# Optimization experiments

Measured on AMD Instinct MI355X. Metric: run time of the kernel, lower is better.

## Reference

```python
import jax, jax.numpy as jnp
import numpy as np

B, N, C, H = 32, 577, 768, 12
D = C // H  # head dim 64
HID = 3072  # hardcoded Mlp hidden
ALPHA = 0.1
EPS = 1e-6


def setup_inputs() -> dict:
    key = jax.random.key(0)
    ks = jax.random.split(key, 8)
    s = 0.02
    return {
        "x": jax.random.normal(ks[0], (B, N, C), jnp.float32),
        "attn_weight": jax.random.uniform(ks[1], (B, N - 1), jnp.float32),
        "ln1_w": jnp.ones((C,), jnp.float32),
        "ln1_b": jnp.zeros((C,), jnp.float32),
        "qkv_w": jax.random.normal(ks[2], (3 * C, C), jnp.float32) * s,
        "qkv_b": jnp.zeros((3 * C,), jnp.float32),
        "proj_w": jax.random.normal(ks[3], (C, C), jnp.float32) * s,
        "proj_b": jnp.zeros((C,), jnp.float32),
        "ln2_w": jnp.ones((C,), jnp.float32),
        "ln2_b": jnp.zeros((C,), jnp.float32),
        "fc1_w": jax.random.normal(ks[4], (HID, C), jnp.float32) * s,
        "fc1_b": jnp.zeros((HID,), jnp.float32),
        "fc2_w": jax.random.normal(ks[5], (C, HID), jnp.float32) * s,
        "fc2_b": jnp.zeros((C,), jnp.float32),
    }


def _ln(x, w, b):
    m = x.mean(-1, keepdims=True)
    v = jnp.var(x, axis=-1, keepdims=True)
    return (x - m) * jax.lax.rsqrt(v + EPS) * w + b


def reference(x, attn_weight, ln1_w, ln1_b, qkv_w, qkv_b, proj_w, proj_b,
              ln2_w, ln2_b, fc1_w, fc1_b, fc2_w, fc2_b):
    h = _ln(x, ln1_w, ln1_b)
    qkv = (h @ qkv_w.T + qkv_b).reshape(B, N, 3, H, D)
    q = qkv[:, :, 0].transpose(0, 2, 1, 3)  # [B,H,N,D]
    k = qkv[:, :, 1].transpose(0, 2, 1, 3)
    v = qkv[:, :, 2].transpose(0, 2, 1, 3)
    scale = D ** -0.5
    attn = jnp.einsum('bhnd,bhmd->bhnm', q, k) * scale  # [B,H,N,N]
    patch_attn = attn[:, :, 0, 1:]  # pre-reweight CLS->patch scores
    # multiplicative reweighting of CLS row (cols 1:) before softmax
    factor = jnp.concatenate(
        [jnp.ones((B, 1), attn.dtype), attn_weight * ALPHA + (1.0 - ALPHA)], axis=-1)
    attn = attn.at[:, :, 0, :].multiply(factor[:, None, :])
    attn = jax.nn.softmax(attn, axis=-1)
    out = jnp.einsum('bhnm,bhmd->bhnd', attn, v)
    out = out.transpose(0, 2, 1, 3).reshape(B, N, C)
    out = out @ proj_w.T + proj_b
    x = x + out
    h2 = _ln(x, ln2_w, ln2_b)
    h2 = jax.nn.gelu(h2 @ fc1_w.T + fc1_b, approximate=False)  # nn.GELU exact
    h2 = h2 @ fc2_w.T + fc2_b
    x = x + h2
    return (x, patch_attn)
```

## Files before the change

kernel.cpp:

```cpp
#include <hip/hip_runtime.h>
#include <hip/hip_bf16.h>
#include <cstdint>

#define BB 32
#define NN 577
#define CC 768
#define HH 12
#define HIDN 3072
#define MROWS (BB*NN)

typedef __attribute__((ext_vector_type(8))) short bf16x8;
typedef __attribute__((ext_vector_type(4))) float f32x4;

__device__ __forceinline__ float b2f(unsigned short u) {
    union { float f; unsigned int i; } x; x.i = ((unsigned int)u) << 16; return x.f;
}
__device__ __forceinline__ unsigned short f2b(float f) {
    union { float f; unsigned int i; } x; x.f = f;
    unsigned int i = x.i;
    i += 0x7fffu + ((i >> 16) & 1u);
    return (unsigned short)(i >> 16);
}

__device__ __forceinline__ void async16(const void* g, void* l) {
    __builtin_amdgcn_global_load_lds(
        (const __attribute__((address_space(1))) uint32_t*)g,
        (__attribute__((address_space(3))) uint32_t*)l, 16, 0, 0);
}

__device__ __forceinline__ float gelu_f(float v) {
    float ax = fabsf(v) * 0.70710678118654752f;
    float t = __builtin_amdgcn_rcpf(1.0f + 0.3275911f * ax);
    float poly = t * (0.254829592f + t * (-0.284496736f + t * (1.421413741f +
                 t * (-1.453152027f + t * 1.061405429f))));
    float e = __expf(-ax * ax);
    float erf_abs = 1.0f - poly * e;
    float erf_v = (v >= 0.f) ? erf_abs : -erf_abs;
    return 0.5f * v * (1.0f + erf_v);
}

__global__ void cvt4(const float* __restrict__ a, int na, unsigned short* __restrict__ oa,
                     const float* __restrict__ b, int nb, unsigned short* __restrict__ ob,
                     const float* __restrict__ c, int nc, unsigned short* __restrict__ oc,
                     const float* __restrict__ d, int nd, unsigned short* __restrict__ od) {
    int stride = gridDim.x * blockDim.x;
    int t = blockIdx.x * blockDim.x + threadIdx.x;
    for (int i = t; i < na; i += stride) oa[i] = f2b(a[i]);
    for (int i = t; i < nb; i += stride) ob[i] = f2b(b[i]);
    for (int i = t; i < nc; i += stride) oc[i] = f2b(c[i]);
    for (int i = t; i < nd; i += stride) od[i] = f2b(d[i]);
}

__global__ __launch_bounds__(256)
void ln_kernel(const float* __restrict__ x, const float* __restrict__ w,
               const float* __restrict__ bsv, unsigned short* __restrict__ out) {
    int row = blockIdx.x;
    const float* xr = x + (size_t)row * CC;
    float v[3]; float s = 0.f, ss = 0.f;
    #pragma unroll
    for (int i = 0; i < 3; ++i) {
        v[i] = xr[threadIdx.x + i * 256];
        s += v[i]; ss += v[i] * v[i];
    }
    int lane = threadIdx.x & 63, wv = threadIdx.x >> 6;
    #pragma unroll
    for (int off = 32; off; off >>= 1) { s += __shfl_down(s, off); ss += __shfl_down(ss, off); }
    __shared__ float rs[4], rss[4];
    __shared__ float mean_s, rstd_s;
    if (lane == 0) { rs[wv] = s; rss[wv] = ss; }
    __syncthreads();
    if (threadIdx.x == 0) {
        float S = rs[0] + rs[1] + rs[2] + rs[3];
        float SS = rss[0] + rss[1] + rss[2] + rss[3];
        float m = S * (1.0f / 768.0f);
        float var = SS * (1.0f / 768.0f) - m * m;
        mean_s = m; rstd_s = rsqrtf(var + 1e-6f);
    }
    __syncthreads();
    float m = mean_s, r = rstd_s;
    #pragma unroll
    for (int i = 0; i < 3; ++i) {
        int c = threadIdx.x + i * 256;
        out[(size_t)row * CC + c] = f2b((v[i] - m) * r * w[c] + bsv[c]);
    }
}

template <int EPI>
__global__ __launch_bounds__(256, 4)
void gemm_bt(const unsigned short* __restrict__ A, const unsigned short* __restrict__ Bw,
             const float* __restrict__ bias, const float* __restrict__ resid,
             unsigned short* __restrict__ outb, float* __restrict__ outf,
             int M, int N, int K) {
    const int NT = gridDim.x;
    const int MT = (M + 127) >> 7;
    int flat = blockIdx.y * NT + blockIdx.x;
    int xcd = flat & 7, s = flat >> 3;
    int n_t = s % NT, mj = s / NT;
    int m_t = xcd + 8 * mj;
    if (m_t >= MT) return;
    const int m0 = m_t * 128, n0 = n_t * 128;

    __shared__ __align__(16) unsigned short As[2][128 * 32];
    __shared__ __align__(16) unsigned short Bs[2][128 * 32];
    const int tid = threadIdx.x;
    const int wave = tid >> 6, lane = tid & 63;
    const int wr = wave >> 1, wc = wave & 1;
    const int quad = lane >> 4, l16 = lane & 15;

    f32x4 acc[4][4] = {};

    const int c0 = tid, c1 = 256 + tid;
    const int row0 = c0 >> 2, seg0 = c0 & 3;
    const int row1 = c1 >> 2, seg1 = c1 & 3;
    int gm0 = m0 + row0; if (gm0 > M - 1) gm0 = M - 1;
    int gm1 = m0 + row1; if (gm1 > M - 1) gm1 = M - 1;
    const unsigned short* a0 = A + (size_t)gm0 * K + seg0 * 8;
    const unsigned short* a1 = A + (size_t)gm1 * K + seg1 * 8;
    const unsigned short* b0 = Bw + (size_t)(n0 + row0) * K + seg0 * 8;
    const unsigned short* b1 = Bw + (size_t)(n0 + row1) * K + seg1 * 8;

    for (int k0 = 0; k0 < K; k0 += 64) {
        #pragma unroll
        for (int p = 0; p < 2; ++p) {
            int kk = k0 + p * 32;
            async16(a0 + kk, &As[p][c0 * 8]);
            async16(a1 + kk, &As[p][c1 * 8]);
            async16(b0 + kk, &Bs[p][c0 * 8]);
            async16(b1 + kk, &Bs[p][c1 * 8]);
        }
        __syncthreads();
        #pragma unroll
        for (int p = 0; p < 2; ++p) {
            bf16x8 bfr[4];
            #pragma unroll
            for (int ni = 0; ni < 4; ++ni)
                bfr[ni] = *(const bf16x8*)&Bs[p][(wc * 64 + ni * 16 + l16) * 32 + quad * 8];
            #pragma unroll
            for (int mi = 0; mi < 4; ++mi) {
                bf16x8 af = *(const bf16x8*)&As[p][(wr * 64 + mi * 16 + l16) * 32 + quad * 8];
                #pragma unroll
                for (int ni = 0; ni < 4; ++ni)
                    acc[mi][ni] = __builtin_amdgcn_mfma_f32_16x16x32_bf16(af, bfr[ni], acc[mi][ni], 0, 0, 0);
            }
        }
        __syncthreads();
    }

    #pragma unroll
    for (int mi = 0; mi < 4; ++mi) {
        #pragma unroll
        for (int r = 0; r < 4; ++r) {
            int grow = m0 + wr * 64 + mi * 16 + quad * 4 + r;
            if (grow >= M) continue;
            #pragma unroll
            for (int ni = 0; ni < 4; ++ni) {
                int gcol = n0 + wc * 64 + ni * 16 + l16;
                float v = acc[mi][ni][r] + bias[gcol];
                size_t idx = (size_t)grow * N + gcol;
                if (EPI == 0) {
                    outb[idx] = f2b(v);
                } else if (EPI == 1) {
                    outb[idx] = f2b(gelu_f(v));
                } else {
                    outf[idx] = resid[idx] + v;
                }
            }
        }
    }
}

__global__ __launch_bounds__(256)
void attn_mfma(const unsigned short* __restrict__ qkv, const float* __restrict__ aw,
               unsigned short* __restrict__ O, float* __restrict__ patch) {
    const int qt = blockIdx.x, h = blockIdx.y, b = blockIdx.z;
    const int tid = threadIdx.x, wv = tid >> 6, lane = tid & 63;
    const int quad = lane >> 4, l16 = lane & 15;

    __shared__ __align__(16) unsigned short Ks[64 * 72];
    __shared__ __align__(16) unsigned short Vt[64 * 72];
    __shared__ __align__(16) unsigned short Pt[4][16 * 72];

    int qrow = qt * 64 + wv * 16 + l16;
    int qclamp = qrow < NN ? qrow : NN - 1;
    const unsigned short* qbase = qkv + (size_t)(b * NN + qclamp) * 2304 + h * 64;
    bf16x8 qf[2];
    qf[0] = *(const bf16x8*)(qbase + quad * 8);
    qf[1] = *(const bf16x8*)(qbase + 32 + quad * 8);
    #pragma unroll
    for (int i = 0; i < 2; ++i) {
        union { bf16x8 v; unsigned short u[8]; } t; t.v = qf[i];
        #pragma unroll
        for (int j = 0; j < 8; ++j) t.u[j] = f2b(b2f(t.u[j]) * 0.125f);
        qf[i] = t.v;
    }

    f32x4 o[4] = {};
    float mst[4], lst[4];
    #pragma unroll
    for (int r = 0; r < 4; ++r) { mst[r] = -1.0e30f; lst[r] = 0.f; }

    for (int kt = 0; kt < 10; ++kt) {
        __syncthreads();
        #pragma unroll
        for (int i = 0; i < 2; ++i) {
            int c = i * 256 + tid;
            int key = c >> 3, seg = c & 7;
            int gk = kt * 64 + key; if (gk >= NN) gk = NN - 1;
            const unsigned short* kb = qkv + (size_t)(b * NN + gk) * 2304 + 768 + h * 64 + seg * 8;
            bf16x8 kv = *(const bf16x8*)kb;
            *(bf16x8*)&Ks[key * 72 + seg * 8] = kv;
            const unsigned short* vb = qkv + (size_t)(b * NN + gk) * 2304 + 1536 + h * 64 + seg * 8;
            bf16x8 vvv = *(const bf16x8*)vb;
            int kg = key >> 3, kl = key & 7;
            int swz = (kg ^ seg) * 8 + kl;
            #pragma unroll
            for (int e = 0; e < 8; ++e)
                Vt[(seg * 8 + e) * 72 + swz] = ((const unsigned short*)&vvv)[e];
        }
        __syncthreads();

        f32x4 s[4];
        #pragma unroll
        for (int ni = 0; ni < 4; ++ni) {
            bf16x8 b0 = *(const bf16x8*)&Ks[(ni * 16 + l16) * 72 + quad * 8];
            bf16x8 b1 = *(const bf16x8*)&Ks[(ni * 16 + l16) * 72 + 32 + quad * 8];
            f32x4 acc = {};
            acc = __builtin_amdgcn_mfma_f32_16x16x32_bf16(qf[0], b0, acc, 0, 0, 0);
            acc = __builtin_amdgcn_mfma_f32_16x16x32_bf16(qf[1], b1, acc, 0, 0, 0);
            s[ni] = acc;
        }

        if (kt == 9) {
            #pragma unroll
            for (int ni = 0; ni < 4; ++ni) {
                if (ni * 16 + l16 != 0) {
                    #pragma unroll
                    for (int r = 0; r < 4; ++r) s[ni][r] = -1.0e30f;
                }
            }
        }

        if (qt == 0 && wv == 0 && quad == 0) {
            #pragma unroll
            for (int ni = 0; ni < 4; ++ni) {
                int gkey = kt * 64 + ni * 16 + l16;
                if (gkey >= 1 && gkey < NN) {
                    patch[(size_t)(b * HH + h) * (NN - 1) + gkey - 1] = s[ni][0];
                    float f = aw[b * (NN - 1) + gkey - 1] * 0.1f + 0.9f;
                    s[ni][0] *= f;
                }
            }
        }

        float al[4];
        #pragma unroll
        for (int r = 0; r < 4; ++r) {
            float tm = fmaxf(fmaxf(s[0][r], s[1][r]), fmaxf(s[2][r], s[3][r]));
            tm = fmaxf(tm, __shfl_xor(tm, 1));
            tm = fmaxf(tm, __shfl_xor(tm, 2));
            tm = fmaxf(tm, __shfl_xor(tm, 4));
            tm = fmaxf(tm, __shfl_xor(tm, 8));
            float nm = fmaxf(mst[r], tm);
            al[r] = __expf(mst[r] - nm);
            mst[r] = nm;
        }
        #pragma unroll
        for (int r = 0; r < 4; ++r) {
            float rs = 0.f;
            #pragma unroll
            for (int ni = 0; ni < 4; ++ni) {
                float p = __expf(s[ni][r] - mst[r]);
                Pt[wv][(quad * 4 + r) * 72 + ni * 16 + l16] = f2b(p);
                rs += p;
            }
            rs += __shfl_xor(rs, 1);
            rs += __shfl_xor(rs, 2);
            rs += __shfl_xor(rs, 4);
            rs += __shfl_xor(rs, 8);
            lst[r] = lst[r] * al[r] + rs;
            #pragma unroll
            for (int ni = 0; ni < 4; ++ni) o[ni][r] *= al[r];
        }

        #pragma unroll
        for (int kc = 0; kc < 2; ++kc) {
            bf16x8 af = *(const bf16x8*)&Pt[wv][l16 * 72 + kc * 32 + quad * 8];
            #pragma unroll
            for (int ni = 0; ni < 4; ++ni) {
                int d = ni * 16 + l16;
                int gs = (kc * 4 + quad) ^ (d >> 3);
                bf16x8 vf = *(const bf16x8*)&Vt[d * 72 + gs * 8];
                o[ni] = __builtin_amdgcn_mfma_f32_16x16x32_bf16(af, vf, o[ni], 0, 0, 0);
            }
        }
    }

    #pragma unroll
    for (int r = 0; r < 4; ++r) {
        float inv = (lst[r] > 0.f) ? __builtin_amdgcn_rcpf(lst[r]) : 0.f;
        int row = qt * 64 + wv * 16 + quad * 4 + r;
        if (row < NN) {
            #pragma unroll
            for (int ni = 0; ni < 4; ++ni)
                O[(size_t)(b * NN + row) * CC + h * 64 + ni * 16 + l16] = f2b(o[ni][r] * inv);
        }
    }
}

extern "C" void kernel_launch(void* const* d_in, const int* in_sizes, int n_in,
                              void* d_out, int out_size, void* d_ws, size_t ws_size,
                              hipStream_t stream) {
    const float* x       = (const float*)d_in[0];
    const float* aw      = (const float*)d_in[1];
    const float* ln1w    = (const float*)d_in[2];
    const float* ln1b    = (const float*)d_in[3];
    const float* qkvw_f  = (const float*)d_in[4];
    const float* qkvb    = (const float*)d_in[5];
    const float* projw_f = (const float*)d_in[6];
    const float* projb   = (const float*)d_in[7];
    const float* ln2w    = (const float*)d_in[8];
    const float* ln2b    = (const float*)d_in[9];
    const float* fc1w_f  = (const float*)d_in[10];
    const float* fc1b    = (const float*)d_in[11];
    const float* fc2w_f  = (const float*)d_in[12];
    const float* fc2b    = (const float*)d_in[13];

    char* ws = (char*)d_ws;
    unsigned short* h_bf  = (unsigned short*)(ws + 0);
    unsigned short* qkv   = (unsigned short*)(ws + 28360704);
    unsigned short* g1    = (unsigned short*)(ws + 0);
    unsigned short* attno = (unsigned short*)(ws + 113442816);
    float*          x1    = (float*)(ws + 141803520);
    unsigned short* h2    = (unsigned short*)(ws + 198524928);
    unsigned short* qkvw  = (unsigned short*)(ws + 226885632);
    unsigned short* projw = (unsigned short*)(ws + 230424576);
    unsigned short* fc1w  = (unsigned short*)(ws + 231604224);
    unsigned short* fc2w  = (unsigned short*)(ws + 236322816);

    float* out_x = (float*)d_out;
    float* out_patch = out_x + (size_t)MROWS * CC;

    cvt4<<<1024, 256, 0, stream>>>(qkvw_f, 2304 * 768, qkvw,
                                   projw_f, 768 * 768, projw,
                                   fc1w_f, 3072 * 768, fc1w,
                                   fc2w_f, 768 * 3072, fc2w);
    ln_kernel<<<MROWS, 256, 0, stream>>>(x, ln1w, ln1b, h_bf);
    gemm_bt<0><<<dim3(18, 152), 256, 0, stream>>>(h_bf, qkvw, qkvb, nullptr, qkv, nullptr,
                                                  MROWS, 2304, 768);
    attn_mfma<<<dim3(10, HH, BB), 256, 0, stream>>>(qkv, aw, attno, out_patch);
    gemm_bt<2><<<dim3(6, 152), 256, 0, stream>>>(attno, projw, projb, x, nullptr, x1,
                                                 MROWS, 768, 768);
    ln_kernel<<<MROWS, 256, 0, stream>>>(x1, ln2w, ln2b, h2);
    gemm_bt<1><<<dim3(24, 152), 256, 0, stream>>>(h2, fc1w, fc1b, nullptr, g1, nullptr,
                                                  MROWS, 3072, 768);
    gemm_bt<2><<<dim3(6, 152), 256, 0, stream>>>(g1, fc2w, fc2b, x1, nullptr, out_x,
                                                 MROWS, 768, 3072);
}
```

Before: 709.5 us.

## Prefetch next K/V tile into registers and compute softmax row sums via MFMA

The attention kernel now loads the next key/value tile into registers while the current tile is being computed, so global load latency overlaps with MFMA work. The per-row softmax denominator is no longer built from shuffle reductions. Instead an extra MFMA against a ones-column accumulates it, which also sums the bf16-rounded probabilities. s_setprio hints are wrapped around the MFMA sections. The prefetch adds register pressure, and the extra MFMA adds matrix work in exchange for removing the shuffles.

Result: faster. 682.7 us (-3.8%).

```diff
diff --git a/kernel.cpp b/kernel.cpp
--- a/kernel.cpp
+++ b/kernel.cpp
@@ -194,32 +194,63 @@
         qf[i] = t.v;
     }
 
+    union { bf16x8 v; unsigned short u[8]; } onesf;
+    #pragma unroll
+    for (int j = 0; j < 8; ++j) onesf.u[j] = (l16 == 0) ? (unsigned short)0x3F80 : (unsigned short)0;
+
     f32x4 o[4] = {};
-    float mst[4], lst[4];
-    #pragma unroll
-    for (int r = 0; r < 4; ++r) { mst[r] = -1.0e30f; lst[r] = 0.f; }
+    f32x4 o5 = {};
+    float mst[4];
+    #pragma unroll
+    for (int r = 0; r < 4; ++r) mst[r] = -1.0e30f;
+
+    int keyc[2], segc[2], swzc[2];
+    const unsigned short* kb_base;
+    const unsigned short* vb_base;
+    {
+        int c0 = tid, c1 = 256 + tid;
+        keyc[0] = c0 >> 3; segc[0] = c0 & 7;
+        keyc[1] = c1 >> 3; segc[1] = c1 & 7;
+        #pragma unroll
+        for (int i = 0; i < 2; ++i) {
+            int kg = keyc[i] >> 3, kl = keyc[i] & 7;
+            swzc[i] = (kg ^ segc[i]) * 8 + kl;
+        }
+        kb_base = qkv + (size_t)b * NN * 2304 + 768 + h * 64;
+        vb_base = qkv + (size_t)b * NN * 2304 + 1536 + h * 64;
+    }
+
+    bf16x8 pk[2], pv[2];
+    #pragma unroll
+    for (int i = 0; i < 2; ++i) {
+        int gk = keyc[i]; if (gk >= NN) gk = NN - 1;
+        pk[i] = *(const bf16x8*)(kb_base + (size_t)gk * 2304 + segc[i] * 8);
+        pv[i] = *(const bf16x8*)(vb_base + (size_t)gk * 2304 + segc[i] * 8);
+    }
 
     for (int kt = 0; kt < 10; ++kt) {
         __syncthreads();
         #pragma unroll
         for (int i = 0; i < 2; ++i) {
-            int c = i * 256 + tid;
-            int key = c >> 3, seg = c & 7;
-            int gk = kt * 64 + key; if (gk >= NN) gk = NN - 1;
-            const unsigned short* kb = qkv + (size_t)(b * NN + gk) * 2304 + 768 + h * 64 + seg * 8;
-            bf16x8 kv = *(const bf16x8*)kb;
-            *(bf16x8*)&Ks[key * 72 + seg * 8] = kv;
-            const unsigned short* vb = qkv + (size_t)(b * NN + gk) * 2304 + 1536 + h * 64 + seg * 8;
-            bf16x8 vvv = *(const bf16x8*)vb;
-            int kg = key >> 3, kl = key & 7;
-            int swz = (kg ^ seg) * 8 + kl;
+            *(bf16x8*)&Ks[keyc[i] * 72 + segc[i] * 8] = pk[i];
+            union { bf16x8 v; unsigned short u[8]; } t; t.v = pv[i];
             #pragma unroll
             for (int e = 0; e < 8; ++e)
-                Vt[(seg * 8 + e) * 72 + swz] = ((const unsigned short*)&vvv)[e];
+                Vt[(segc[i] * 8 + e) * 72 + swzc[i]] = t.u[e];
         }
         __syncthreads();
 
+        if (kt < 9) {
+            #pragma unroll
+            for (int i = 0; i < 2; ++i) {
+                int gk = (kt + 1) * 64 + keyc[i]; if (gk >= NN) gk = NN - 1;
+                pk[i] = *(const bf16x8*)(kb_base + (size_t)gk * 2304 + segc[i] * 8);
+                pv[i] = *(const bf16x8*)(vb_base + (size_t)gk * 2304 + segc[i] * 8);
+            }
+        }
+
         f32x4 s[4];
+        __builtin_amdgcn_s_setprio(1);
         #pragma unroll
         for (int ni = 0; ni < 4; ++ni) {
             bf16x8 b0 = *(const bf16x8*)&Ks[(ni * 16 + l16) * 72 + quad * 8];
@@ -229,6 +260,7 @@
             acc = __builtin_amdgcn_mfma_f32_16x16x32_bf16(qf[1], b1, acc, 0, 0, 0);
             s[ni] = acc;
         }
+        __builtin_amdgcn_s_setprio(0);
 
         if (kt == 9) {
             #pragma unroll
@@ -266,22 +298,17 @@
         }
         #pragma unroll
         for (int r = 0; r < 4; ++r) {
-            float rs = 0.f;
             #pragma unroll
             for (int ni = 0; ni < 4; ++ni) {
                 float p = __expf(s[ni][r] - mst[r]);
                 Pt[wv][(quad * 4 + r) * 72 + ni * 16 + l16] = f2b(p);
-                rs += p;
-            }
-            rs += __shfl_xor(rs, 1);
-            rs += __shfl_xor(rs, 2);
-            rs += __shfl_xor(rs, 4);
-            rs += __shfl_xor(rs, 8);
-            lst[r] = lst[r] * al[r] + rs;
+            }
             #pragma unroll
             for (int ni = 0; ni < 4; ++ni) o[ni][r] *= al[r];
-        }
-
+            o5[r] *= al[r];
+        }
+
+        __builtin_amdgcn_s_setprio(1);
         #pragma unroll
         for (int kc = 0; kc < 2; ++kc) {
             bf16x8 af = *(const bf16x8*)&Pt[wv][l16 * 72 + kc * 32 + quad * 8];
@@ -292,12 +319,15 @@
                 bf16x8 vf = *(const bf16x8*)&Vt[d * 72 + gs * 8];
                 o[ni] = __builtin_amdgcn_mfma_f32_16x16x32_bf16(af, vf, o[ni], 0, 0, 0);
             }
-        }
+            o5 = __builtin_amdgcn_mfma_f32_16x16x32_bf16(af, onesf.v, o5, 0, 0, 0);
+        }
+        __builtin_amdgcn_s_setprio(0);
     }
 
     #pragma unroll
     for (int r = 0; r < 4; ++r) {
-        float inv = (lst[r] > 0.f) ? __builtin_amdgcn_rcpf(lst[r]) : 0.f;
+        float lr = __shfl(o5[r], quad << 4);
+        float inv = (lr > 0.f) ? __builtin_amdgcn_rcpf(lr) : 0.f;
         int row = qt * 64 + wv * 16 + quad * 4 + r;
         if (row < NN) {
             #pragma unroll
```
